# Kernel tuning notes

Hardware: AMD Instinct MI355X
Metric: run time of the kernel (lower is better)

Reference implementation:

```python
import jax, jax.numpy as jnp
import numpy as np

D, H, M, FF = 1024, 16, 64, 4096
B, N, C = 8, 1024, 256


def setup_inputs() -> dict:
    key = jax.random.key(0)
    it = iter(jax.random.split(key, 24))
    def nrm(shape, s):
        return jax.random.normal(next(it), shape, dtype=jnp.float32) * s
    z = lambda *s: jnp.zeros(s, jnp.float32)
    inp = {
        'point_tokens': nrm((B, N, D), 1.0),
        'context_tokens': nrm((B, C, D), 1.0),
        'inducing': nrm((1, M, D), 0.02),
    }
    for p in ('ti', 'tp'):  # to_induced / to_points MHA
        for w in ('Wq', 'Wk', 'Wv', 'Wo'):
            inp[f'{p}_{w}'] = nrm((D, D), 0.02)
        for b in ('bq', 'bk', 'bv', 'bo'):
            inp[f'{p}_{b}'] = z(D)
    for p in ('iff', 'pff'):  # induced_ff / point_ff: LN + Linear + GELU + Linear
        inp[f'{p}_g'] = jnp.ones(D, jnp.float32); inp[f'{p}_b'] = z(D)
        inp[f'{p}_W1'] = nrm((D, FF), 0.02); inp[f'{p}_b1'] = z(FF)
        inp[f'{p}_W2'] = nrm((FF, D), 0.02); inp[f'{p}_b2'] = z(D)
    inp['ni_g'] = jnp.ones(D, jnp.float32); inp['ni_b'] = z(D)
    inp['np_g'] = jnp.ones(D, jnp.float32); inp['np_b'] = z(D)
    return inp


def layernorm(x, g, b, eps=1e-5):
    mu = x.mean(-1, keepdims=True)
    var = ((x - mu) ** 2).mean(-1, keepdims=True)
    return (x - mu) * jax.lax.rsqrt(var + eps) * g + b


def ffn(x, g, b0, W1, b1, W2, b2):
    h = layernorm(x, g, b0)
    h = jax.nn.gelu(h @ W1 + b1, approximate=False)  # torch nn.GELU default = exact erf
    return h @ W2 + b2


def mha(q, kv, Wq, bq, Wk, bk, Wv, bv, Wo, bo):
    # torch nn.MultiheadAttention semantics (batch_first, dropout=0, need_weights=True)
    Bq, Lq, Dm = q.shape
    Lk = kv.shape[1]
    hd = Dm // H
    Q = (q @ Wq + bq).reshape(Bq, Lq, H, hd)
    K = (kv @ Wk + bk).reshape(Bq, Lk, H, hd)
    V = (kv @ Wv + bv).reshape(Bq, Lk, H, hd)
    scores = jnp.einsum('bqhd,bkhd->bhqk', Q, K) / jnp.sqrt(jnp.float32(hd))
    probs = jax.nn.softmax(scores, axis=-1)
    out = jnp.einsum('bhqk,bkhd->bqhd', probs, V).reshape(Bq, Lq, Dm)
    return out @ Wo + bo, probs.mean(axis=1)  # head-averaged weights (need_weights default)


def reference(point_tokens, context_tokens, inducing,
              ti_Wq, ti_bq, ti_Wk, ti_bk, ti_Wv, ti_bv, ti_Wo, ti_bo,
              tp_Wq, tp_bq, tp_Wk, tp_bk, tp_Wv, tp_bv, tp_Wo, tp_bo,
              iff_g, iff_b, iff_W1, iff_b1, iff_W2, iff_b2,
              pff_g, pff_b, pff_W1, pff_b1, pff_W2, pff_b2,
              ni_g, ni_b, np_g, np_b):
    b = point_tokens.shape[0]
    induced = jnp.broadcast_to(inducing, (b, inducing.shape[1], inducing.shape[2]))
    kv = jnp.concatenate([context_tokens, point_tokens], axis=1)
    ia, _ = mha(induced, kv, ti_Wq, ti_bq, ti_Wk, ti_bk, ti_Wv, ti_bv, ti_Wo, ti_bo)
    induced = layernorm(induced + ia, ni_g, ni_b)
    induced = induced + ffn(induced, iff_g, iff_b, iff_W1, iff_b1, iff_W2, iff_b2)
    kv2 = jnp.concatenate([context_tokens, induced], axis=1)
    pa, w2 = mha(point_tokens, kv2, tp_Wq, tp_bq, tp_Wk, tp_bk, tp_Wv, tp_bv, tp_Wo, tp_bo)
    pts = layernorm(point_tokens + pa, np_g, np_b)
    pts = pts + ffn(pts, pff_g, pff_b, pff_W1, pff_b1, pff_W2, pff_b2)
    probs = jnp.clip(w2, 1e-8, None)
    entropy = (-(probs * jnp.log(probs)).sum(axis=-1)).mean()  # detached side output
    return pts, entropy
```

## Files before the change

kernel.cpp:

```cpp
#include <hip/hip_runtime.h>
#include <hip/hip_bf16.h>
#include <math.h>

typedef unsigned short ushort_t;
typedef __attribute__((ext_vector_type(8))) short short8;
typedef __attribute__((ext_vector_type(4))) float f32x4;

static __device__ __forceinline__ ushort_t f2b(float f){
  union{float f;unsigned u;}a; a.f=f;
  unsigned r = a.u + 0x7fffu + ((a.u>>16)&1u);
  return (ushort_t)(r>>16);
}
static __device__ __forceinline__ float b2f(ushort_t u){
  union{unsigned u;float f;}a; a.u=((unsigned)u)<<16; return a.f;
}

#define GLDS16(g,l) __builtin_amdgcn_global_load_lds((const __attribute__((address_space(1))) void*)(const void*)(g), (__attribute__((address_space(3))) void*)(void*)(l), 16, 0, 0)

template<bool GELU, int RES>
__global__ __launch_bounds__(512)
void gemm256(const ushort_t* __restrict__ A, const ushort_t* __restrict__ Bt,
             const float* __restrict__ bias, const void* __restrict__ Res,
             float* __restrict__ Cf, ushort_t* __restrict__ Cb,
             int M, int N, int K, int lda, int ldb, int ldres, int ldcf, int ldcb,
             int nb0,
             long sA0, long sA1, long sB0, long sB1, long sR0, long sR1,
             long sCf0, long sCf1, long sCb0, long sCb1, float scale)
{
  const int z = blockIdx.z;
  const int zb0 = z % nb0, zb1 = z / nb0;
  A  += zb0*sA0 + zb1*sA1;
  Bt += zb0*sB0 + zb1*sB1;
  const float* RpF = 0; const ushort_t* RpB = 0;
  if (RES==1) RpF = (const float*)Res + zb0*sR0 + zb1*sR1;
  if (RES==2) RpB = (const ushort_t*)Res + zb0*sR0 + zb1*sR1;
  if (Cf) Cf += zb0*sCf0 + zb1*sCf1;
  if (Cb) Cb += zb0*sCb0 + zb1*sCb1;

  const int gx = gridDim.x;
  const int nwg = gx * gridDim.y;
  const int orig = blockIdx.y*gx + blockIdx.x;
  const int q8 = nwg >> 3, r8 = nwg & 7;
  const int xcd = orig & 7, ii = orig >> 3;
  const int wg = (xcd < r8 ? xcd*(q8+1) : r8*(q8+1) + (xcd-r8)*q8) + ii;
  const int bm = (wg / gx)*256, bn = (wg % gx)*128;

  __shared__ __align__(16) char AsR[3][32768];
  __shared__ __align__(16) char BsR[3][16384];

  const int tid = threadIdx.x, lane = tid&63, w = tid>>6;
  const int wr = w>>1, wc = w&1;
  const int lr = lane&15, g16 = (lane>>4)*16;
  const int rxor = (lr&7)<<4;

  f32x4 acc[4][4] = {};

  const int colElem = ((lane&7) ^ ((lane>>3)&7)) << 3;
  const int srRow = w*8 + (lane>>3);
  const ushort_t* pAst[4];
  const ushort_t* pBst[2];
#pragma unroll
  for (int a=0;a<4;a++){
    long r = min((long)(bm + a*64 + srRow), (long)M-1);
    pAst[a] = A + r*lda + colElem;
  }
#pragma unroll
  for (int b=0;b<2;b++){
    long r = min((long)(bn + b*64 + srRow), (long)N-1);
    pBst[b] = Bt + r*ldb + colElem;
  }

  const int aOff = (wr*64 + lr)*128;
  const int bOff = (wc*64 + lr)*128;
  const int NT = K >> 6;

#define STAGE256(Ad, Bd, ktEl) do { \
    GLDS16(pAst[0] + (ktEl), (Ad) + 0*8192 + w*1024); \
    GLDS16(pAst[1] + (ktEl), (Ad) + 1*8192 + w*1024); \
    GLDS16(pAst[2] + (ktEl), (Ad) + 2*8192 + w*1024); \
    GLDS16(pAst[3] + (ktEl), (Ad) + 3*8192 + w*1024); \
    GLDS16(pBst[0] + (ktEl), (Bd) + 0*8192 + w*1024); \
    GLDS16(pBst[1] + (ktEl), (Bd) + 1*8192 + w*1024); \
  } while(0)

  char *Ac = AsR[0], *An1 = AsR[1], *An2 = AsR[2];
  char *Bc = BsR[0], *Bn1 = BsR[1], *Bn2 = BsR[2];

  STAGE256(Ac, Bc, 0);
  if (NT > 1) STAGE256(An1, Bn1, 64);
  asm volatile("s_waitcnt vmcnt(6)" ::: "memory");
  __builtin_amdgcn_s_barrier();

  for (int t=0; t<NT; ++t){
    short8 a0[4], b0[4], a1[4], b1[4];

#pragma unroll
    for (int m=0;m<4;m++) a0[m] = *(const short8*)(Ac + aOff + m*2048 + (g16 ^ rxor));
#pragma unroll
    for (int n=0;n<4;n++) b0[n] = *(const short8*)(Bc + bOff + n*2048 + (g16 ^ rxor));
    if (t+2 < NT) STAGE256(An2, Bn2, (long)(t+2)<<6);
    __builtin_amdgcn_s_barrier();
    asm volatile("s_waitcnt lgkmcnt(0)" ::: "memory");
    __builtin_amdgcn_sched_barrier(0);
    __builtin_amdgcn_s_setprio(1);
#pragma unroll
    for (int m=0;m<4;m++)
#pragma unroll
      for (int n=0;n<4;n++)
        acc[m][n] = __builtin_amdgcn_mfma_f32_16x16x32_bf16(a0[m], b0[n], acc[m][n],0,0,0);
    __builtin_amdgcn_s_setprio(0);
    __builtin_amdgcn_sched_barrier(0);
    __builtin_amdgcn_s_barrier();

#pragma unroll
    for (int m=0;m<4;m++) a1[m] = *(const short8*)(Ac + aOff + m*2048 + ((64 + g16) ^ rxor));
#pragma unroll
    for (int n=0;n<4;n++) b1[n] = *(const short8*)(Bc + bOff + n*2048 + ((64 + g16) ^ rxor));
    __builtin_amdgcn_s_barrier();
    asm volatile("s_waitcnt lgkmcnt(0)" ::: "memory");
    __builtin_amdgcn_sched_barrier(0);
    __builtin_amdgcn_s_setprio(1);
#pragma unroll
    for (int m=0;m<4;m++)
#pragma unroll
      for (int n=0;n<4;n++)
        acc[m][n] = __builtin_amdgcn_mfma_f32_16x16x32_bf16(a1[m], b1[n], acc[m][n],0,0,0);
    __builtin_amdgcn_s_setprio(0);
    __builtin_amdgcn_sched_barrier(0);
    if (t+2 < NT)      { asm volatile("s_waitcnt vmcnt(6)" ::: "memory"); }
    else if (t+1 < NT) { asm volatile("s_waitcnt vmcnt(0)" ::: "memory"); }
    __builtin_amdgcn_s_barrier();
    char* ta = Ac; Ac = An1; An1 = An2; An2 = ta;
    char* tb = Bc; Bc = Bn1; Bn1 = Bn2; Bn2 = tb;
  }
#undef STAGE256

  const int orow = bm + wr*64, ocol = bn + wc*64;
  const int rsub = (lane>>4)*4;
#pragma unroll
  for (int n=0;n<4;n++){
    const int col = ocol + n*16 + lr;
    if (col >= N) continue;
    const float bv = bias ? bias[col] : 0.f;
#pragma unroll
    for (int m=0;m<4;m++){
#pragma unroll
      for (int i=0;i<4;i++){
        const int row = orow + m*16 + rsub + i;
        if (row >= M) continue;
        float v = acc[m][n][i]*scale + bv;
        if (GELU) v = 0.5f*v*(1.f + erff(v*0.70710678118654752f));
        if (RES==1) v += RpF[(long)row*ldres + col];
        if (RES==2) v += b2f(RpB[(long)row*ldres + col]);
        if (Cf) Cf[(long)row*ldcf + col] = v;
        if (Cb) Cb[(long)row*ldcb + col] = f2b(v);
      }
    }
  }
}

template<bool GELU, int RES>
__global__ __launch_bounds__(256)
void gemm_bt(const ushort_t* __restrict__ A, const ushort_t* __restrict__ Bt,
             const float* __restrict__ bias, const void* __restrict__ Res,
             float* __restrict__ Cf, ushort_t* __restrict__ Cb,
             int M, int N, int K, int lda, int ldb, int ldres, int ldcf, int ldcb,
             int nb0,
             long sA0, long sA1, long sB0, long sB1, long sR0, long sR1,
             long sCf0, long sCf1, long sCb0, long sCb1, float scale, int resMask)
{
  const int z = blockIdx.z;
  const int b0 = z % nb0, b1 = z / nb0;
  A  += b0*sA0 + b1*sA1;
  Bt += b0*sB0 + b1*sB1;
  const float* RpF = 0; const ushort_t* RpB = 0;
  if (RES==1) RpF = (const float*)Res + b0*sR0 + b1*sR1;
  if (RES==2) RpB = (const ushort_t*)Res + b0*sR0 + b1*sR1;
  if (Cf) Cf += b0*sCf0 + b1*sCf1;
  if (Cb) Cb += b0*sCb0 + b1*sCb1;

  const int gx = gridDim.x;
  const int nwg = gx * gridDim.y;
  const int orig = blockIdx.y*gx + blockIdx.x;
  const int q8 = nwg >> 3, r8 = nwg & 7;
  const int xcd = orig & 7, ii = orig >> 3;
  const int wg = (xcd < r8 ? xcd*(q8+1) : r8*(q8+1) + (xcd-r8)*q8) + ii;
  const int bm = (wg / gx)*128, bn = (wg % gx)*128;

  __shared__ __align__(16) ushort_t As[2][4096];
  __shared__ __align__(16) ushort_t Bs[2][4096];
  const int tid = threadIdx.x, lane = tid&63, wave = tid>>6;
  const int wr = wave>>1, wc = wave&1;

  f32x4 acc[4][4] = {};

  const int c0 = wave*64 + lane;
  const int c1 = c0 + 256;
  const long rA0 = min(bm + (c0>>2), M-1);
  const long rA1 = min(bm + (c1>>2), M-1);
  const long rB0 = min(bn + (c0>>2), N-1);
  const long rB1 = min(bn + (c1>>2), N-1);
  const ushort_t* pA0 = A + rA0*lda + (c0&3)*8;
  const ushort_t* pA1 = A + rA1*lda + (c1&3)*8;
  const ushort_t* pB0 = Bt + rB0*ldb + (c0&3)*8;
  const ushort_t* pB1 = Bt + rB1*ldb + (c1&3)*8;
  const int ldsOff = wave*512;

  const int lr = lane&15, lk = (lane>>4)*8;

#define STAGE(buf, kt) do { \
    GLDS16(pA0 + (kt), &As[buf][ldsOff]); \
    GLDS16(pA1 + (kt), &As[buf][2048 + ldsOff]); \
    GLDS16(pB0 + (kt), &Bs[buf][ldsOff]); \
    GLDS16(pB1 + (kt), &Bs[buf][2048 + ldsOff]); \
  } while(0)

  STAGE(0, 0);
  __syncthreads();
  int cur = 0;
  for (int kt = 0; kt < K; kt += 32) {
    if (kt + 32 < K) STAGE(cur^1, kt+32);
    short8 af[4], bfv[4];
#pragma unroll
    for (int m=0;m<4;m++) af[m]  = *(const short8*)(&As[cur][(wr*64+m*16+lr)*32 + lk]);
#pragma unroll
    for (int n=0;n<4;n++) bfv[n] = *(const short8*)(&Bs[cur][(wc*64+n*16+lr)*32 + lk]);
#pragma unroll
    for (int m=0;m<4;m++)
#pragma unroll
      for (int n=0;n<4;n++)
        acc[m][n] = __builtin_amdgcn_mfma_f32_16x16x32_bf16(af[m], bfv[n], acc[m][n], 0, 0, 0);
    __syncthreads();
    cur ^= 1;
  }
#undef STAGE

  const int orow = bm + wr*64, ocol = bn + wc*64;
  const int rsub = (lane>>4)*4;
#pragma unroll
  for (int n=0;n<4;n++){
    const int col = ocol + n*16 + lr;
    if (col >= N) continue;
    const float bv = bias ? bias[col] : 0.f;
#pragma unroll
    for (int m=0;m<4;m++){
#pragma unroll
      for (int i=0;i<4;i++){
        const int row = orow + m*16 + rsub + i;
        if (row >= M) continue;
        float v = acc[m][n][i]*scale + bv;
        if (GELU) v = 0.5f*v*(1.f + erff(v*0.70710678118654752f));
        if (RES==1) v += RpF[(long)(row & resMask)*ldres + col];
        if (RES==2) v += b2f(RpB[(long)(row & resMask)*ldres + col]);
        if (Cf) Cf[(long)row*ldcf + col] = v;
        if (Cb) Cb[(long)row*ldcb + col] = f2b(v);
      }
    }
  }
}

template<bool WRITEP>
__global__ __launch_bounds__(256)
void fattn_k(const ushort_t* __restrict__ Qb, const ushort_t* __restrict__ KVb,
             const ushort_t* __restrict__ Vtb, ushort_t* __restrict__ Ob,
             ushort_t* __restrict__ Pb,
             int LK, int ldkv, int qRowsPerB, int oRowsPerB, float scale)
{
  const int z = blockIdx.z, b = z >> 4, h = z & 15;
  const int qt = blockIdx.x;
  const int tid = threadIdx.x, lane = tid & 63, wave = tid >> 6;
  const int lr = lane & 15, g = lane >> 4;

  __shared__ __align__(16) ushort_t Kls[64*68];
  __shared__ __align__(16) ushort_t Vtls[64*68];
  __shared__ __align__(16) ushort_t Pls[64*68];

  const long qrow = (long)b*qRowsPerB + qt*64 + wave*16 + lr;
  const short8 aq0 = *(const short8*)(Qb + qrow*1024 + h*64 + g*8);
  const short8 aq1 = *(const short8*)(Qb + qrow*1024 + h*64 + 32 + g*8);

  const ushort_t* Kbase = KVb + (long)b*LK*ldkv + h*64;
  const ushort_t* Vtbase = Vtb + (long)(b*16+h)*64*LK;

  const int ntiles = LK >> 6;
  const int r0 = tid>>3, d0c = (tid&7)*8;
  const int r1 = r0 + 32;

  float m[4] = {-3e30f,-3e30f,-3e30f,-3e30f};
  float l[4] = {0.f,0.f,0.f,0.f};

  for (int t=0; t<ntiles; ++t){
    __syncthreads();
    { short8 v0 = *(const short8*)(Kbase + (long)(t*64 + r0)*ldkv + d0c);
      short8 v1 = *(const short8*)(Kbase + (long)(t*64 + r1)*ldkv + d0c);
      *(short8*)(Kls + r0*68 + d0c) = v0;
      *(short8*)(Kls + r1*68 + d0c) = v1; }
    __syncthreads();
    f32x4 s[4];
#pragma unroll
    for(int n=0;n<4;n++){
      s[n] = (f32x4){0.f,0.f,0.f,0.f};
      short8 bk0 = *(const short8*)(Kls + (n*16+lr)*68 + g*8);
      short8 bk1 = *(const short8*)(Kls + (n*16+lr)*68 + 32 + g*8);
      s[n] = __builtin_amdgcn_mfma_f32_16x16x32_bf16(aq0, bk0, s[n],0,0,0);
      s[n] = __builtin_amdgcn_mfma_f32_16x16x32_bf16(aq1, bk1, s[n],0,0,0);
    }
#pragma unroll
    for(int i=0;i<4;i++){
      float mx = fmaxf(fmaxf(s[0][i],s[1][i]), fmaxf(s[2][i],s[3][i])) * scale;
#pragma unroll
      for(int o2=1;o2<16;o2<<=1) mx = fmaxf(mx, __shfl_xor(mx,o2));
      float mnew = fmaxf(m[i], mx);
      float sum = __expf(s[0][i]*scale-mnew)+__expf(s[1][i]*scale-mnew)
                + __expf(s[2][i]*scale-mnew)+__expf(s[3][i]*scale-mnew);
#pragma unroll
      for(int o2=1;o2<16;o2<<=1) sum += __shfl_xor(sum,o2);
      l[i] = l[i]*__expf(m[i]-mnew) + sum;
      m[i] = mnew;
    }
  }
  float invl[4];
#pragma unroll
  for(int i=0;i<4;i++) invl[i] = 1.f/l[i];

  f32x4 o[4];
#pragma unroll
  for(int n=0;n<4;n++) o[n] = (f32x4){0.f,0.f,0.f,0.f};

  long pbase = 0;
  if (WRITEP) pbase = ((long)(b*16+h)*1024 + qt*64 + wave*16)*320 + lr;

  for (int t=0; t<ntiles; ++t){
    __syncthreads();
    { short8 v0 = *(const short8*)(Kbase + (long)(t*64 + r0)*ldkv + d0c);
      short8 v1 = *(const short8*)(Kbase + (long)(t*64 + r1)*ldkv + d0c);
      short8 w0 = *(const short8*)(Vtbase + (long)r0*LK + t*64 + d0c);
      short8 w1 = *(const short8*)(Vtbase + (long)r1*LK + t*64 + d0c);
      *(short8*)(Kls + r0*68 + d0c) = v0;
      *(short8*)(Kls + r1*68 + d0c) = v1;
      *(short8*)(Vtls + r0*68 + d0c) = w0;
      *(short8*)(Vtls + r1*68 + d0c) = w1; }
    __syncthreads();
    f32x4 s[4];
#pragma unroll
    for(int n=0;n<4;n++){
      s[n] = (f32x4){0.f,0.f,0.f,0.f};
      short8 bk0 = *(const short8*)(Kls + (n*16+lr)*68 + g*8);
      short8 bk1 = *(const short8*)(Kls + (n*16+lr)*68 + 32 + g*8);
      s[n] = __builtin_amdgcn_mfma_f32_16x16x32_bf16(aq0, bk0, s[n],0,0,0);
      s[n] = __builtin_amdgcn_mfma_f32_16x16x32_bf16(aq1, bk1, s[n],0,0,0);
    }
#pragma unroll
    for(int n=0;n<4;n++){
#pragma unroll
      for(int i=0;i<4;i++){
        float e = __expf(s[n][i]*scale - m[i]);
        Pls[(wave*16 + g*4 + i)*68 + n*16 + lr] = f2b(e);
        if (WRITEP) Pb[pbase + (long)(g*4+i)*320 + t*64 + n*16] = f2b(e*invl[i]);
      }
    }
    short8 pa0 = *(const short8*)(Pls + (wave*16+lr)*68 + g*8);
    short8 pa1 = *(const short8*)(Pls + (wave*16+lr)*68 + 32 + g*8);
#pragma unroll
    for(int nd=0; nd<4; nd++){
      short8 vb0 = *(const short8*)(Vtls + (nd*16+lr)*68 + g*8);
      short8 vb1 = *(const short8*)(Vtls + (nd*16+lr)*68 + 32 + g*8);
      o[nd] = __builtin_amdgcn_mfma_f32_16x16x32_bf16(pa0, vb0, o[nd],0,0,0);
      o[nd] = __builtin_amdgcn_mfma_f32_16x16x32_bf16(pa1, vb1, o[nd],0,0,0);
    }
  }
  const long orow0 = (long)b*oRowsPerB + qt*64 + wave*16 + g*4;
#pragma unroll
  for(int nd=0;nd<4;nd++)
#pragma unroll
    for(int i=0;i<4;i++)
      Ob[(orow0+i)*1024 + h*64 + nd*16 + lr] = f2b(o[nd][i]*invl[i]);
}

__global__ __launch_bounds__(256)
void tcvt_k(const float* __restrict__ src, ushort_t* __restrict__ dst, int R, int C)
{
  __shared__ float t[32][33];
  int c0 = blockIdx.x*32, r0 = blockIdx.y*32;
  int tx = threadIdx.x & 31, ty = threadIdx.x >> 5;
  for (int i=ty;i<32;i+=8){ int r=r0+i, c=c0+tx; t[i][tx] = (r<R && c<C) ? src[(long)r*C + c] : 0.f; }
  __syncthreads();
  for (int i=ty;i<32;i+=8){ int c=c0+i, r=r0+tx; if (c<C && r<R) dst[(long)c*R + r] = f2b(t[tx][i]); }
}

__global__ __launch_bounds__(256)
void cvt_rows_k(const float* __restrict__ src, ushort_t* __restrict__ dst,
                long total, int R, long dstBS, long dstRO)
{
  long e = ((long)blockIdx.x*256 + threadIdx.x)*4;
  if (e >= total) return;
  long rc = e >> 10; int c = (int)(e & 1023);
  int r = (int)(rc % R); long b = rc / R;
  float4 v = *(const float4*)(src + e);
  ushort4 o; o.x=f2b(v.x); o.y=f2b(v.y); o.z=f2b(v.z); o.w=f2b(v.w);
  *(ushort4*)(dst + (b*dstBS + dstRO + r)*1024 + c) = o;
}

__global__ __launch_bounds__(256)
void vtrans_k(const ushort_t* __restrict__ V, ushort_t* __restrict__ Vt,
              int Lk, int ldv, int coloff)
{
  int b = blockIdx.z, h = blockIdx.y, k0 = blockIdx.x*32;
  __shared__ ushort_t t[32][65];
  int tx = threadIdx.x & 63, ty = threadIdx.x >> 6;
  for (int i=ty;i<32;i+=4) t[i][tx] = V[((long)b*Lk + k0 + i)*ldv + coloff + h*64 + tx];
  __syncthreads();
  int kk = threadIdx.x & 31, n0 = threadIdx.x >> 5;
  for (int n=n0;n<64;n+=8) Vt[((long)(b*16+h)*64 + n)*Lk + k0 + kk] = t[kk][n];
}

__global__ __launch_bounds__(256)
void ln2x_k(const float* __restrict__ x,
            const float* __restrict__ g1, const float* __restrict__ b1,
            const float* __restrict__ g2, const float* __restrict__ b2,
            float* __restrict__ y1f, ushort_t* __restrict__ y1b, ushort_t* __restrict__ y2b)
{
  const long row = blockIdx.x;
  int tid = threadIdx.x, lane = tid&63, wave = tid>>6;
  __shared__ float red[8], red2[8];
  float4 v = ((const float4*)(x + row*1024))[tid];
  float s = v.x+v.y+v.z+v.w;
  for (int o=32;o;o>>=1) s += __shfl_down(s,o);
  if (lane==0) red[wave]=s;
  __syncthreads();
  float mean = (red[0]+red[1]+red[2]+red[3])*(1.f/1024.f);
  float d0=v.x-mean, d1=v.y-mean, d2=v.z-mean, d3=v.w-mean;
  float q = d0*d0+d1*d1+d2*d2+d3*d3;
  for (int o=32;o;o>>=1) q += __shfl_down(q,o);
  if (lane==0) red[4+wave]=q;
  __syncthreads();
  float var = (red[4]+red[5]+red[6]+red[7])*(1.f/1024.f);
  float rs = rsqrtf(var+1e-5f);
  float4 gg=((const float4*)g1)[tid], bb=((const float4*)b1)[tid];
  float y0=d0*rs*gg.x+bb.x, y1v=d1*rs*gg.y+bb.y, y2v=d2*rs*gg.z+bb.z, y3=d3*rs*gg.w+bb.w;
  if (y1f) ((float4*)(y1f+row*1024))[tid] = make_float4(y0,y1v,y2v,y3);
  if (y1b){ ushort4 o4; o4.x=f2b(y0); o4.y=f2b(y1v); o4.z=f2b(y2v); o4.w=f2b(y3);
            ((ushort4*)(y1b+row*1024))[tid]=o4; }
  float s2 = y0+y1v+y2v+y3;
  for (int o=32;o;o>>=1) s2 += __shfl_down(s2,o);
  if (lane==0) red2[wave]=s2;
  __syncthreads();
  float mean2 = (red2[0]+red2[1]+red2[2]+red2[3])*(1.f/1024.f);
  float e0=y0-mean2,e1=y1v-mean2,e2=y2v-mean2,e3=y3-mean2;
  float q2 = e0*e0+e1*e1+e2*e2+e3*e3;
  for (int o=32;o;o>>=1) q2 += __shfl_down(q2,o);
  if (lane==0) red2[4+wave]=q2;
  __syncthreads();
  float var2 = (red2[4]+red2[5]+red2[6]+red2[7])*(1.f/1024.f);
  float rs2 = rsqrtf(var2+1e-5f);
  float4 g2v=((const float4*)g2)[tid], b2v=((const float4*)b2)[tid];
  ushort4 o4;
  o4.x=f2b(e0*rs2*g2v.x+b2v.x); o4.y=f2b(e1*rs2*g2v.y+b2v.y);
  o4.z=f2b(e2*rs2*g2v.z+b2v.z); o4.w=f2b(e3*rs2*g2v.w+b2v.w);
  ((ushort4*)(y2b+row*1024))[tid]=o4;
}

__global__ __launch_bounds__(256)
void w2ent_k(const ushort_t* __restrict__ P, float* __restrict__ rowent)
{
  int wid = (int)((blockIdx.x*256 + threadIdx.x) >> 6);
  int lane = threadIdx.x & 63;
  int b = wid >> 10, q = wid & 1023;
  const ushort_t* base = P + ((long)(b*16)*1024 + q)*320;
  float acc = 0.f;
#pragma unroll
  for (int j=0;j<5;j++){
    int k = j*64 + lane;
    float s = 0.f;
#pragma unroll
    for (int h=0;h<16;h++) s += b2f(base[(long)h*327680 + k]);
    float p = fmaxf(s*(1.f/16.f), 1e-8f);
    acc += p*__logf(p);
  }
  for (int o=32;o;o>>=1) acc += __shfl_down(acc, o);
  if (lane==0) rowent[wid] = acc;
}

__global__ __launch_bounds__(256)
void entfin_k(const float* __restrict__ rowent, float* __restrict__ out)
{
  float s = 0.f;
  for (int i=threadIdx.x;i<8192;i+=256) s += rowent[i];
  __shared__ float red[4];
  for (int o=32;o;o>>=1) s += __shfl_down(s,o);
  if ((threadIdx.x&63)==0) red[threadIdx.x>>6]=s;
  __syncthreads();
  if (threadIdx.x==0) out[0] = -(red[0]+red[1]+red[2]+red[3]) * (1.f/8192.f);
}

__global__ void dbg_k(float* out, float a){ out[0] = -12345.f; out[1] = a; }

static void gemm(hipStream_t s, int mode,
                 const void* A, const void* Bt, const float* bias, const void* Res,
                 void* Cf, void* Cb,
                 int M, int N, int K, int lda, int ldb, int ldres, int ldcf, int ldcb,
                 int nz, int nb0,
                 long sA0, long sA1, long sB0, long sB1, long sR0, long sR1,
                 long sCf0, long sCf1, long sCb0, long sCb1, float scale, int resMask)
{
  dim3 g((N+127)/128, (M+127)/128, nz), b(256,1,1);
#define ARGS (const ushort_t*)A,(const ushort_t*)Bt,bias,Res,(float*)Cf,(ushort_t*)Cb,M,N,K,lda,ldb,ldres,ldcf,ldcb,nb0,sA0,sA1,sB0,sB1,sR0,sR1,sCf0,sCf1,sCb0,sCb1,scale,resMask
  if      (mode == 1) gemm_bt<true ,0><<<g,b,0,s>>>(ARGS);
  else if (mode == 2) gemm_bt<false,1><<<g,b,0,s>>>(ARGS);
  else if (mode == 3) gemm_bt<false,2><<<g,b,0,s>>>(ARGS);
  else                gemm_bt<false,0><<<g,b,0,s>>>(ARGS);
#undef ARGS
}

static void g256(hipStream_t s, int mode,
                 const void* A, const void* Bt, const float* bias, const void* Res,
                 void* Cf, void* Cb,
                 int M, int N, int K, int lda, int ldb, int ldres, int ldcf, int ldcb,
                 int nz, int nb0,
                 long sA0, long sA1, long sB0, long sB1, long sR0, long sR1,
                 long sCf0, long sCf1, long sCb0, long sCb1, float scale)
{
  dim3 g((N+127)/128, (M+255)/256, nz), b(512,1,1);
#define ARGS (const ushort_t*)A,(const ushort_t*)Bt,bias,Res,(float*)Cf,(ushort_t*)Cb,M,N,K,lda,ldb,ldres,ldcf,ldcb,nb0,sA0,sA1,sB0,sB1,sR0,sR1,sCf0,sCf1,sCb0,sCb1,scale
  if      (mode == 1) gemm256<true ,0><<<g,b,0,s>>>(ARGS);
  else if (mode == 2) gemm256<false,1><<<g,b,0,s>>>(ARGS);
  else if (mode == 3) gemm256<false,2><<<g,b,0,s>>>(ARGS);
  else                gemm256<false,0><<<g,b,0,s>>>(ARGS);
#undef ARGS
}

extern "C" void kernel_launch(void* const* d_in, const int* in_sizes, int n_in,
                              void* d_out, int out_size, void* d_ws, size_t ws_size,
                              hipStream_t stream)
{
  const float* ptsIn = (const float*)d_in[0];
  const float* ctx   = (const float*)d_in[1];
  const float* induc = (const float*)d_in[2];
  const float* tiW[4]={(const float*)d_in[3],(const float*)d_in[4],(const float*)d_in[5],(const float*)d_in[6]};
  const float* tib[4]={(const float*)d_in[7],(const float*)d_in[8],(const float*)d_in[9],(const float*)d_in[10]};
  const float* tpW[4]={(const float*)d_in[11],(const float*)d_in[12],(const float*)d_in[13],(const float*)d_in[14]};
  const float* tpb[4]={(const float*)d_in[15],(const float*)d_in[16],(const float*)d_in[17],(const float*)d_in[18]};
  const float* iff_g=(const float*)d_in[19]; const float* iff_b=(const float*)d_in[20];
  const float* iffW1=(const float*)d_in[21]; const float* iff_b1=(const float*)d_in[22];
  const float* iffW2=(const float*)d_in[23]; const float* iff_b2=(const float*)d_in[24];
  const float* pff_g=(const float*)d_in[25]; const float* pff_b=(const float*)d_in[26];
  const float* pffW1=(const float*)d_in[27]; const float* pff_b1=(const float*)d_in[28];
  const float* pffW2=(const float*)d_in[29]; const float* pff_b2=(const float*)d_in[30];
  const float* ni_g=(const float*)d_in[31]; const float* ni_b=(const float*)d_in[32];
  const float* np_g=(const float*)d_in[33]; const float* np_b=(const float*)d_in[34];
  float* outF = (float*)d_out;

  char* ws = (char*)d_ws;
  size_t off = 0;
  auto alloc = [&](size_t bytes){ off=(off+255)&~(size_t)255; size_t o=off; off+=bytes; return o; };
  auto sub = [&](size_t& pp, size_t bytes){ pp=(pp+255)&~(size_t)255; size_t o=pp; pp+=bytes; return o; };

  size_t o_tiQw  = alloc(1024L*1024*2);
  size_t o_tiKVw = alloc(2048L*1024*2);
  size_t o_tiOw  = alloc(1024L*1024*2);
  size_t o_tpQw  = alloc(1024L*1024*2);
  size_t o_tpKVw = alloc(2048L*1024*2);
  size_t o_tpOw  = alloc(1024L*1024*2);
  size_t o_iffW1t = alloc(4096L*1024*2);
  size_t o_iffW2t = alloc(4096L*1024*2);
  size_t o_pffW1t = alloc(4096L*1024*2);
  size_t o_pffW2t = alloc(4096L*1024*2);
  size_t o_bti  = alloc(2048*4);
  size_t o_btp  = alloc(2048*4);
  size_t o_indb = alloc(64L*1024*2);
  size_t o_kv   = alloc(10240L*1024*2);
  size_t o_kv2  = alloc(2560L*1024*2);
  size_t o_rowent = alloc(8192*4);
  off=(off+255)&~(size_t)255;
  size_t arena = off;

  size_t p = arena;
  size_t o_Qti     = sub(p, 64L*1024*2);
  size_t o_KVti    = sub(p, 10240L*2048*2);
  size_t o_Vtti    = sub(p, 8192L*1280*2);
  size_t o_attnOti = sub(p, 512L*1024*2);
  size_t o_t1      = sub(p, 512L*1024*4);
  size_t o_ind1    = sub(p, 512L*1024*4);
  size_t o_h0i     = sub(p, 512L*1024*2);
  size_t o_h1i     = sub(p, 512L*4096*2);
  size_t need1 = p;
  p = arena;
  size_t o_attnOtp = sub(p, 8192L*1024*2);
  size_t shared = p;
  size_t o_Qtp  = sub(p, 8192L*1024*2);
  size_t o_KVtp = sub(p, 2560L*2048*2);
  size_t o_Vttp = sub(p, 8192L*320*2);
  size_t o_P    = sub(p, 8L*16*1024*320*2);
  size_t need3 = p;
  p = shared;
  size_t o_t2   = sub(p, 8192L*1024*4);
  size_t o_pts1 = sub(p, 8192L*1024*2);
  size_t o_h0p  = sub(p, 8192L*1024*2);
  size_t o_h1p  = sub(p, 8192L*4096*2);
  size_t need4 = p;

  size_t need = need1;
  if (need3>need) need=need3;
  if (need4>need) need=need4;
  if (need > ws_size){ dbg_k<<<1,1,0,stream>>>(outF, (float)(need>>20)); return; }

#define WP(o) ((void*)(ws + (o)))
#define BP(o) ((ushort_t*)(ws + (o)))
#define FP(o) ((float*)(ws + (o)))

  tcvt_k<<<dim3(32,32),256,0,stream>>>(tiW[0], BP(o_tiQw), 1024, 1024);
  tcvt_k<<<dim3(32,32),256,0,stream>>>(tiW[1], BP(o_tiKVw), 1024, 1024);
  tcvt_k<<<dim3(32,32),256,0,stream>>>(tiW[2], BP(o_tiKVw) + 1024L*1024, 1024, 1024);
  tcvt_k<<<dim3(32,32),256,0,stream>>>(tiW[3], BP(o_tiOw), 1024, 1024);
  tcvt_k<<<dim3(32,32),256,0,stream>>>(tpW[0], BP(o_tpQw), 1024, 1024);
  tcvt_k<<<dim3(32,32),256,0,stream>>>(tpW[1], BP(o_tpKVw), 1024, 1024);
  tcvt_k<<<dim3(32,32),256,0,stream>>>(tpW[2], BP(o_tpKVw) + 1024L*1024, 1024, 1024);
  tcvt_k<<<dim3(32,32),256,0,stream>>>(tpW[3], BP(o_tpOw), 1024, 1024);
  tcvt_k<<<dim3(128,32),256,0,stream>>>(iffW1, BP(o_iffW1t), 1024, 4096);
  tcvt_k<<<dim3(32,128),256,0,stream>>>(iffW2, BP(o_iffW2t), 4096, 1024);
  tcvt_k<<<dim3(128,32),256,0,stream>>>(pffW1, BP(o_pffW1t), 1024, 4096);
  tcvt_k<<<dim3(32,128),256,0,stream>>>(pffW2, BP(o_pffW2t), 4096, 1024);
  hipMemcpyAsync(WP(o_bti), (const void*)tib[1], 1024*4, hipMemcpyDeviceToDevice, stream);
  hipMemcpyAsync((void*)(ws+o_bti+1024*4), (const void*)tib[2], 1024*4, hipMemcpyDeviceToDevice, stream);
  hipMemcpyAsync(WP(o_btp), (const void*)tpb[1], 1024*4, hipMemcpyDeviceToDevice, stream);
  hipMemcpyAsync((void*)(ws+o_btp+1024*4), (const void*)tpb[2], 1024*4, hipMemcpyDeviceToDevice, stream);

  cvt_rows_k<<<2048,256,0,stream>>>(ctx,   BP(o_kv),  8L*256*1024, 256, 1280, 0);
  cvt_rows_k<<<8192,256,0,stream>>>(ptsIn, BP(o_kv),  8L*1024*1024, 1024, 1280, 256);
  cvt_rows_k<<<64,256,0,stream>>>(induc,   BP(o_indb), 64L*1024, 64, 64, 0);
  cvt_rows_k<<<2048,256,0,stream>>>(ctx,   BP(o_kv2), 8L*256*1024, 256, 320, 0);

  gemm(stream,0, WP(o_indb), WP(o_tiQw), tib[0], 0, 0, WP(o_Qti),
       64,1024,1024, 1024,1024,0,0,1024, 1,1, 0,0,0,0,0,0,0,0,0,0, 1.f,-1);
  g256(stream,0, WP(o_kv), WP(o_tiKVw), FP(o_bti), 0, 0, WP(o_KVti),
       10240,2048,1024, 1024,1024,0,0,2048, 1,1, 0,0,0,0,0,0,0,0,0,0, 1.f);
  vtrans_k<<<dim3(40,16,8),256,0,stream>>>(BP(o_KVti), BP(o_Vtti), 1280, 2048, 1024);
  fattn_k<false><<<dim3(1,1,128),256,0,stream>>>(BP(o_Qti), BP(o_KVti), BP(o_Vtti),
       BP(o_attnOti), (ushort_t*)0, 1280, 2048, 0, 64, 0.125f);
  gemm(stream,2, WP(o_attnOti), WP(o_tiOw), tib[3], (const void*)induc, WP(o_t1), 0,
       512,1024,1024, 1024,1024,1024,1024,0, 1,1, 0,0,0,0,0,0,0,0,0,0, 1.f,63);
  ln2x_k<<<512,256,0,stream>>>(FP(o_t1), ni_g, ni_b, iff_g, iff_b, FP(o_ind1), 0, BP(o_h0i));
  gemm(stream,1, WP(o_h0i), WP(o_iffW1t), iff_b1, 0, 0, WP(o_h1i),
       512,4096,1024, 1024,1024,0,0,4096, 1,1, 0,0,0,0,0,0,0,0,0,0, 1.f,-1);
  gemm(stream,2, WP(o_h1i), WP(o_iffW2t), iff_b2, WP(o_ind1), 0, BP(o_kv2) + 262144,
       64,1024,4096, 4096,4096,1024,0,1024, 8,8,
       262144,0, 0,0, 65536,0, 0,0, 327680,0, 1.f,-1);

  g256(stream,0, BP(o_kv) + 262144, WP(o_tpQw), tpb[0], 0, 0, WP(o_Qtp),
       1024,1024,1024, 1024,1024,0,0,1024, 8,8,
       1310720,0, 0,0, 0,0, 0,0, 1048576,0, 1.f);
  g256(stream,0, WP(o_kv2), WP(o_tpKVw), FP(o_btp), 0, 0, WP(o_KVtp),
       2560,2048,1024, 1024,1024,0,0,2048, 1,1, 0,0,0,0,0,0,0,0,0,0, 1.f);
  vtrans_k<<<dim3(10,16,8),256,0,stream>>>(BP(o_KVtp), BP(o_Vttp), 320, 2048, 1024);
  fattn_k<true><<<dim3(16,1,128),256,0,stream>>>(BP(o_Qtp), BP(o_KVtp), BP(o_Vttp),
       BP(o_attnOtp), BP(o_P), 320, 2048, 1024, 1024, 0.125f);
  w2ent_k<<<2048,256,0,stream>>>(BP(o_P), FP(o_rowent));
  entfin_k<<<1,256,0,stream>>>(FP(o_rowent), outF + (out_size-1));
  g256(stream,2, WP(o_attnOtp), WP(o_tpOw), tpb[3], (const void*)ptsIn, WP(o_t2), 0,
       8192,1024,1024, 1024,1024,1024,1024,0, 1,1, 0,0,0,0,0,0,0,0,0,0, 1.f);
  ln2x_k<<<8192,256,0,stream>>>(FP(o_t2), np_g, np_b, pff_g, pff_b, 0, BP(o_pts1), BP(o_h0p));
  g256(stream,1, WP(o_h0p), WP(o_pffW1t), pff_b1, 0, 0, WP(o_h1p),
       8192,4096,1024, 1024,1024,0,0,4096, 1,1, 0,0,0,0,0,0,0,0,0,0, 1.f);
  g256(stream,3, WP(o_h1p), WP(o_pffW2t), pff_b2, WP(o_pts1), outF, 0,
       8192,1024,4096, 4096,4096,1024,1024,0, 1,1, 0,0,0,0,0,0,0,0,0,0, 1.f);

#undef WP
#undef BP
#undef FP
}
```

Measured before the change: 912.2 us.

## Enlarge big GEMM tile to 256x256 with double-buffered LDS staging

Replaces the 256x128 triple-buffered GEMM kernel with a 256x256 tile kernel. Each of 8 waves now computes 128x64 using 8x4 accumulators, and the kernel uses two LDS buffers with plain __syncthreads instead of the hand-tuned barrier/waitcnt/setprio schedule. The goal is more operand reuse per loaded byte and fewer workgroups. The costs are higher register pressure (launch_bounds 512,2 with 128 accumulator floats), 128KB of LDS, fewer blocks for the smaller GEMMs, and the loss of the fine-grained load/MFMA interleaving.

```diff
diff --git a/kernel.cpp b/kernel.cpp
--- a/kernel.cpp
+++ b/kernel.cpp
@@ -18,14 +18,14 @@
 #define GLDS16(g,l) __builtin_amdgcn_global_load_lds((const __attribute__((address_space(1))) void*)(const void*)(g), (__attribute__((address_space(3))) void*)(void*)(l), 16, 0, 0)
 
 template<bool GELU, int RES>
-__global__ __launch_bounds__(512)
-void gemm256(const ushort_t* __restrict__ A, const ushort_t* __restrict__ Bt,
-             const float* __restrict__ bias, const void* __restrict__ Res,
-             float* __restrict__ Cf, ushort_t* __restrict__ Cb,
-             int M, int N, int K, int lda, int ldb, int ldres, int ldcf, int ldcb,
-             int nb0,
-             long sA0, long sA1, long sB0, long sB1, long sR0, long sR1,
-             long sCf0, long sCf1, long sCb0, long sCb1, float scale)
+__global__ __launch_bounds__(512, 2)
+void gemm256q(const ushort_t* __restrict__ A, const ushort_t* __restrict__ Bt,
+              const float* __restrict__ bias, const void* __restrict__ Res,
+              float* __restrict__ Cf, ushort_t* __restrict__ Cb,
+              int M, int N, int K, int lda, int ldb, int ldres, int ldcf, int ldcb,
+              int nb0,
+              long sA0, long sA1, long sB0, long sB1, long sR0, long sR1,
+              long sCf0, long sCf1, long sCb0, long sCb1, float scale)
 {
   const int z = blockIdx.z;
   const int zb0 = z % nb0, zb1 = z / nb0;
@@ -43,107 +43,93 @@
   const int q8 = nwg >> 3, r8 = nwg & 7;
   const int xcd = orig & 7, ii = orig >> 3;
   const int wg = (xcd < r8 ? xcd*(q8+1) : r8*(q8+1) + (xcd-r8)*q8) + ii;
-  const int bm = (wg / gx)*256, bn = (wg % gx)*128;
-
-  __shared__ __align__(16) char AsR[3][32768];
-  __shared__ __align__(16) char BsR[3][16384];
+  const int bm = (wg / gx)*256, bn = (wg % gx)*256;
+
+  __shared__ __align__(16) char As[2][32768];
+  __shared__ __align__(16) char Bs[2][32768];
 
   const int tid = threadIdx.x, lane = tid&63, w = tid>>6;
-  const int wr = w>>1, wc = w&1;
-  const int lr = lane&15, g16 = (lane>>4)*16;
-  const int rxor = (lr&7)<<4;
-
-  f32x4 acc[4][4] = {};
+  const int wr = w>>2, wc = w&3;
+  const int lr = lane&15, g = lane>>4;
+  const int e7 = lr & 7;
+
+  f32x4 acc[8][4] = {};
 
   const int colElem = ((lane&7) ^ ((lane>>3)&7)) << 3;
   const int srRow = w*8 + (lane>>3);
   const ushort_t* pAst[4];
-  const ushort_t* pBst[2];
+  const ushort_t* pBst[4];
 #pragma unroll
   for (int a=0;a<4;a++){
     long r = min((long)(bm + a*64 + srRow), (long)M-1);
     pAst[a] = A + r*lda + colElem;
   }
 #pragma unroll
-  for (int b=0;b<2;b++){
+  for (int b=0;b<4;b++){
     long r = min((long)(bn + b*64 + srRow), (long)N-1);
     pBst[b] = Bt + r*ldb + colElem;
   }
 
-  const int aOff = (wr*64 + lr)*128;
-  const int bOff = (wc*64 + lr)*128;
   const int NT = K >> 6;
 
-#define STAGE256(Ad, Bd, ktEl) do { \
+#define STG256(Ad, Bd, ktEl) do { \
     GLDS16(pAst[0] + (ktEl), (Ad) + 0*8192 + w*1024); \
     GLDS16(pAst[1] + (ktEl), (Ad) + 1*8192 + w*1024); \
     GLDS16(pAst[2] + (ktEl), (Ad) + 2*8192 + w*1024); \
     GLDS16(pAst[3] + (ktEl), (Ad) + 3*8192 + w*1024); \
     GLDS16(pBst[0] + (ktEl), (Bd) + 0*8192 + w*1024); \
     GLDS16(pBst[1] + (ktEl), (Bd) + 1*8192 + w*1024); \
+    GLDS16(pBst[2] + (ktEl), (Bd) + 2*8192 + w*1024); \
+    GLDS16(pBst[3] + (ktEl), (Bd) + 3*8192 + w*1024); \
   } while(0)
 
-  char *Ac = AsR[0], *An1 = AsR[1], *An2 = AsR[2];
-  char *Bc = BsR[0], *Bn1 = BsR[1], *Bn2 = BsR[2];
-
-  STAGE256(Ac, Bc, 0);
-  if (NT > 1) STAGE256(An1, Bn1, 64);
-  asm volatile("s_waitcnt vmcnt(6)" ::: "memory");
-  __builtin_amdgcn_s_barrier();
+  STG256(As[0], Bs[0], 0);
+  __syncthreads();
 
   for (int t=0; t<NT; ++t){
-    short8 a0[4], b0[4], a1[4], b1[4];
-
-#pragma unroll
-    for (int m=0;m<4;m++) a0[m] = *(const short8*)(Ac + aOff + m*2048 + (g16 ^ rxor));
-#pragma unroll
-    for (int n=0;n<4;n++) b0[n] = *(const short8*)(Bc + bOff + n*2048 + (g16 ^ rxor));
-    if (t+2 < NT) STAGE256(An2, Bn2, (long)(t+2)<<6);
-    __builtin_amdgcn_s_barrier();
-    asm volatile("s_waitcnt lgkmcnt(0)" ::: "memory");
-    __builtin_amdgcn_sched_barrier(0);
-    __builtin_amdgcn_s_setprio(1);
-#pragma unroll
-    for (int m=0;m<4;m++)
-#pragma unroll
-      for (int n=0;n<4;n++)
-        acc[m][n] = __builtin_amdgcn_mfma_f32_16x16x32_bf16(a0[m], b0[n], acc[m][n],0,0,0);
-    __builtin_amdgcn_s_setprio(0);
-    __builtin_amdgcn_sched_barrier(0);
-    __builtin_amdgcn_s_barrier();
-
-#pragma unroll
-    for (int m=0;m<4;m++) a1[m] = *(const short8*)(Ac + aOff + m*2048 + ((64 + g16) ^ rxor));
-#pragma unroll
-    for (int n=0;n<4;n++) b1[n] = *(const short8*)(Bc + bOff + n*2048 + ((64 + g16) ^ rxor));
-    __builtin_amdgcn_s_barrier();
-    asm volatile("s_waitcnt lgkmcnt(0)" ::: "memory");
-    __builtin_amdgcn_sched_barrier(0);
-    __builtin_amdgcn_s_setprio(1);
-#pragma unroll
-    for (int m=0;m<4;m++)
-#pragma unroll
-      for (int n=0;n<4;n++)
-        acc[m][n] = __builtin_amdgcn_mfma_f32_16x16x32_bf16(a1[m], b1[n], acc[m][n],0,0,0);
-    __builtin_amdgcn_s_setprio(0);
-    __builtin_amdgcn_sched_barrier(0);
-    if (t+2 < NT)      { asm volatile("s_waitcnt vmcnt(6)" ::: "memory"); }
-    else if (t+1 < NT) { asm volatile("s_waitcnt vmcnt(0)" ::: "memory"); }
-    __builtin_amdgcn_s_barrier();
-    char* ta = Ac; Ac = An1; An1 = An2; An2 = ta;
-    char* tb = Bc; Bc = Bn1; Bn1 = Bn2; Bn2 = tb;
-  }
-#undef STAGE256
-
-  const int orow = bm + wr*64, ocol = bn + wc*64;
-  const int rsub = (lane>>4)*4;
+    const char* Ab = As[t&1];
+    const char* Bb = Bs[t&1];
+    char* An = As[(t&1)^1];
+    char* Bn = Bs[(t&1)^1];
+
+    short8 bf[8];
+#pragma unroll
+    for (int n=0;n<4;n++)
+#pragma unroll
+      for (int s=0;s<2;s++)
+        bf[n*2+s] = *(const short8*)(Bb + (wc*64 + n*16 + lr)*128 + (((g + 4*s) ^ e7) << 4));
+
+    if (t+1 < NT) STG256(An, Bn, (long)(t+1)<<6);
+
+#pragma unroll
+    for (int mq=0; mq<4; mq++){
+      short8 af[4];
+#pragma unroll
+      for (int mm=0;mm<2;mm++)
+#pragma unroll
+        for (int s=0;s<2;s++)
+          af[mm*2+s] = *(const short8*)(Ab + (wr*128 + (mq*2+mm)*16 + lr)*128 + (((g + 4*s) ^ e7) << 4));
+#pragma unroll
+      for (int mm=0;mm<2;mm++)
+#pragma unroll
+        for (int n=0;n<4;n++)
+#pragma unroll
+        for (int s=0;s<2;s++)
+          acc[mq*2+mm][n] = __builtin_amdgcn_mfma_f32_16x16x32_bf16(af[mm*2+s], bf[n*2+s], acc[mq*2+mm][n],0,0,0);
+    }
+    __syncthreads();
+  }
+#undef STG256
+
+  const int orow = bm + wr*128, ocol = bn + wc*64;
+  const int rsub = g*4;
 #pragma unroll
   for (int n=0;n<4;n++){
     const int col = ocol + n*16 + lr;
     if (col >= N) continue;
     const float bv = bias ? bias[col] : 0.f;
 #pragma unroll
-    for (int m=0;m<4;m++){
+    for (int m=0;m<8;m++){
 #pragma unroll
       for (int i=0;i<4;i++){
         const int row = orow + m*16 + rsub + i;
@@ -520,12 +506,12 @@
                  long sA0, long sA1, long sB0, long sB1, long sR0, long sR1,
                  long sCf0, long sCf1, long sCb0, long sCb1, float scale)
 {
-  dim3 g((N+127)/128, (M+255)/256, nz), b(512,1,1);
+  dim3 g((N+255)/256, (M+255)/256, nz), b(512,1,1);
 #define ARGS (const ushort_t*)A,(const ushort_t*)Bt,bias,Res,(float*)Cf,(ushort_t*)Cb,M,N,K,lda,ldb,ldres,ldcf,ldcb,nb0,sA0,sA1,sB0,sB1,sR0,sR1,sCf0,sCf1,sCb0,sCb1,scale
-  if      (mode == 1) gemm256<true ,0><<<g,b,0,s>>>(ARGS);
-  else if (mode == 2) gemm256<false,1><<<g,b,0,s>>>(ARGS);
-  else if (mode == 3) gemm256<false,2><<<g,b,0,s>>>(ARGS);
-  else                gemm256<false,0><<<g,b,0,s>>>(ARGS);
+  if      (mode == 1) gemm256q<true ,0><<<g,b,0,s>>>(ARGS);
+  else if (mode == 2) gemm256q<false,1><<<g,b,0,s>>>(ARGS);
+  else if (mode == 3) gemm256q<false,2><<<g,b,0,s>>>(ARGS);
+  else                gemm256q<false,0><<<g,b,0,s>>>(ARGS);
 #undef ARGS
 }
 
```

Measured after the change: 0.9999 ms. +9.6%, slower.
